# Kernel tuning notes

Hardware: AMD Instinct MI355X
Metric: run time of the kernel (lower is better)

Reference implementation:

```python
import jax, jax.numpy as jnp
import numpy as np

B, T, C = 2, 2048, 2048
HK, HV, DK, DV, KW = 16, 32, 128, 128, 4
KEY_DIM = HK * DK          # 2048
VAL_DIM = HV * DV          # 4096
QKV_DIM = 2 * KEY_DIM + VAL_DIM  # 8192
REPEAT = HV // HK
EPS = 1e-6


def setup_inputs() -> dict:
    key = jax.random.key(0)
    ks = jax.random.split(key, 12)
    s = 0.02
    return {
        "x": jax.random.normal(ks[0], (B, T, C), jnp.float32),
        "positions": jnp.arange(B * T, dtype=jnp.int64).reshape(B, T) % T,
        "W_qkv": jax.random.normal(ks[1], (QKV_DIM, C), jnp.float32) * s,
        "W_z": jax.random.normal(ks[2], (VAL_DIM, C), jnp.float32) * s,
        "W_b": jax.random.normal(ks[3], (HV, C), jnp.float32) * s,
        "W_a": jax.random.normal(ks[4], (HV, C), jnp.float32) * s,
        "conv_w": jax.random.normal(ks[5], (QKV_DIM, 1, KW), jnp.float32) * 0.3,
        "dt_bias": jnp.ones((HV,), jnp.float32),
        "A_log": jnp.log(jax.random.uniform(ks[6], (HV,), jnp.float32, 0.01, 16.0)),
        "norm_w": jnp.ones((DV,), jnp.float32),
        "W_out": jax.random.normal(ks[7], (C, VAL_DIM), jnp.float32) * s,
    }


def _forward(x, W_qkv, W_z, W_b, W_a, conv_w, dt_bias, A_log, norm_w, W_out):
    qkv = x @ W_qkv.T                                # [B,T,QKV_DIM]
    z = (x @ W_z.T).reshape(B, T, HV, DV)
    b = x @ W_b.T                                    # [B,T,HV]
    a = x @ W_a.T                                    # [B,T,HV]

    # depthwise causal conv1d (left pad KW-1), then SiLU
    qkv_c = jnp.transpose(qkv, (0, 2, 1))            # [B,QKV_DIM,T]
    qkv_c = jax.lax.conv_general_dilated(
        qkv_c, conv_w, window_strides=(1,), padding=[(KW - 1, 0)],
        dimension_numbers=("NCH", "OIH", "NCH"), feature_group_count=QKV_DIM)
    qkv = jax.nn.silu(jnp.transpose(qkv_c, (0, 2, 1)))

    q, k, v = jnp.split(qkv, [KEY_DIM, 2 * KEY_DIM], axis=-1)
    q = q.reshape(B, T, HK, DK)
    k = k.reshape(B, T, HK, DK)
    v = v.reshape(B, T, HV, DV)
    q = q / jnp.maximum(jnp.linalg.norm(q, axis=-1, keepdims=True), 1e-12)
    k = k / jnp.maximum(jnp.linalg.norm(k, axis=-1, keepdims=True), 1e-12)
    if REPEAT > 1:
        q = jnp.repeat(q, REPEAT, axis=2)            # [B,T,HV,DK]
        k = jnp.repeat(k, REPEAT, axis=2)

    beta = jax.nn.sigmoid(b)                         # [B,T,HV]
    g = -jnp.exp(A_log) * jax.nn.softplus(a + dt_bias)  # [B,T,HV]

    # gated delta-rule recurrence over time (lax.scan, time-major)
    def step(state, inp):
        g_t, beta_t, k_t, v_t, q_t = inp             # [B,HV], [B,HV], [B,HV,DK], [B,HV,DV], [B,HV,DK]
        state = jnp.exp(g_t)[..., None, None] * state \
            + beta_t[..., None, None] * (k_t[..., :, None] * v_t[..., None, :])
        out_t = jnp.einsum("bhk,bhkv->bhv", q_t, state)
        return state, out_t

    tm = lambda u: jnp.moveaxis(u, 1, 0)
    state0 = jnp.zeros((B, HV, DK, DV), x.dtype)
    _, out = jax.lax.scan(step, state0, (tm(g), tm(beta), tm(k), tm(v), tm(q)))
    out = jnp.moveaxis(out, 0, 1)                    # [B,T,HV,DV]

    # gated RMSNorm per head: RMSNorm(out) * silu(z)
    o = out.astype(jnp.float32)
    o = o * jax.lax.rsqrt(jnp.mean(o * o, axis=-1, keepdims=True) + EPS)
    o = (norm_w * o) * jax.nn.silu(z.astype(jnp.float32))
    o = o.astype(x.dtype).reshape(B, T, VAL_DIM)
    return o @ W_out.T                               # [B,T,C]


def reference(x, positions, W_qkv, W_z, W_b, W_a, conv_w, dt_bias, A_log, norm_w, W_out):
    del positions  # unused by the module's math
    return _forward(x, W_qkv, W_z, W_b, W_a, conv_w, dt_bias, A_log, norm_w, W_out)
```

## Files before the change

kernel.cpp:

```cpp
#include <hip/hip_runtime.h>

typedef unsigned short u16;
typedef unsigned int u32;
typedef __attribute__((ext_vector_type(8))) short short8;
typedef __attribute__((ext_vector_type(8))) _Float16 half8;
typedef __attribute__((ext_vector_type(4))) float f32x4;

#define NB 2
#define NT 2048
#define NC 2048
#define NHV 32
#define VALD 4096
#define NBT 4096
#define CL 64
#define NCH (NT / CL)

#define GL16(gp, lp) __builtin_amdgcn_global_load_lds( \
    (const __attribute__((address_space(1))) unsigned int*)(gp), \
    (__attribute__((address_space(3))) unsigned int*)(lp), 16, 0, 0)

static __device__ __forceinline__ float bf2f(u16 u) {
  union { u32 u; float f; } x; x.u = ((u32)u) << 16; return x.f;
}
static __device__ __forceinline__ u16 f2bf(float f) {
  union { float f; u32 u; } x; x.f = f;
  u32 r = x.u + 0x7fffu + ((x.u >> 16) & 1u);
  return (u16)(r >> 16);
}
static __device__ __forceinline__ u16 f2h(float f) {
  union { _Float16 h; u16 u; } c; c.h = (_Float16)f; return c.u;
}
static __device__ __forceinline__ float h2f(u16 u) {
  union { u16 u; _Float16 h; } c; c.u = u; return (float)c.h;
}
static __device__ __forceinline__ float sigm(float x) { return 1.0f / (1.0f + __expf(-x)); }
static __device__ __forceinline__ int ldsoff(int row, int c8) {
  return row * 48 + ((c8 ^ ((row >> 2) & 3)) << 3);
}

__global__ void k_sentinel(float* out) { out[0] = 1.0e6f; }

__global__ __launch_bounds__(256) void k_cvtx(const float* __restrict__ in, u16* __restrict__ hi,
                                              u16* __restrict__ lo, u16* __restrict__ h16, int n4) {
  int i = blockIdx.x * 256 + threadIdx.x;
  if (i >= n4) return;
  float4 v = ((const float4*)in)[i];
  ushort4 h, l, p;
  h.x = f2bf(v.x); l.x = f2bf(v.x - bf2f(h.x)); p.x = f2h(v.x);
  h.y = f2bf(v.y); l.y = f2bf(v.y - bf2f(h.y)); p.y = f2h(v.y);
  h.z = f2bf(v.z); l.z = f2bf(v.z - bf2f(h.z)); p.z = f2h(v.z);
  h.w = f2bf(v.w); l.w = f2bf(v.w - bf2f(h.w)); p.w = f2h(v.w);
  ((ushort4*)hi)[i] = h;
  ((ushort4*)lo)[i] = l;
  ((ushort4*)h16)[i] = p;
}

__global__ __launch_bounds__(256) void k_cvt16(const float* __restrict__ in, u16* __restrict__ out, int n4) {
  int i = blockIdx.x * 256 + threadIdx.x;
  if (i >= n4) return;
  float4 v = ((const float4*)in)[i];
  ushort4 o;
  o.x = f2h(v.x); o.y = f2h(v.y); o.z = f2h(v.z); o.w = f2h(v.w);
  ((ushort4*)out)[i] = o;
}

__global__ __launch_bounds__(256) void k_wba(const float* __restrict__ Wb, const float* __restrict__ Wa,
                                             u16* __restrict__ hi, u16* __restrict__ lo) {
  int i = blockIdx.x * 256 + threadIdx.x;
  int r = i >> 11, c = i & 2047;
  float v = 0.f;
  if (r < 32) v = Wb[r * 2048 + c];
  else if (r < 64) v = Wa[(r - 32) * 2048 + c];
  u16 h = f2bf(v);
  hi[i] = h;
  lo[i] = f2bf(v - bf2f(h));
}

__global__ __launch_bounds__(256) void k_gemm_bf3(const u16* __restrict__ Ahg, const u16* __restrict__ Alg,
                                                  const u16* __restrict__ Bhg, const u16* __restrict__ Blg,
                                                  float* __restrict__ C0, int M, int N, int K) {
  __shared__ __align__(16) u16 As_h[128 * 48];
  __shared__ __align__(16) u16 As_l[128 * 48];
  __shared__ __align__(16) u16 Bs_h[128 * 48];
  __shared__ __align__(16) u16 Bs_l[128 * 48];
  const int tid = threadIdx.x;
  const int lane = tid & 63, wave = tid >> 6;
  const int wr = wave >> 1, wc = wave & 1;
  const int l15 = lane & 15, l16 = lane >> 4;
  const int row0 = blockIdx.y * 128, col0 = blockIdx.x * 128;
  const int sr = tid >> 1, sk = (tid & 1) * 16;
  const int c0 = sk >> 3;
  const int w0 = ldsoff(sr, c0), w1 = ldsoff(sr, c0 + 1);
  f32x4 acc[4][4] = {};
  for (int k0 = 0; k0 < K; k0 += 32) {
    const size_t aoff = (size_t)(row0 + sr) * K + k0 + sk;
    const size_t boff = (size_t)(col0 + sr) * K + k0 + sk;
    *(short8*)&As_h[w0] = *(const short8*)&Ahg[aoff];
    *(short8*)&As_h[w1] = *(const short8*)&Ahg[aoff + 8];
    *(short8*)&As_l[w0] = *(const short8*)&Alg[aoff];
    *(short8*)&As_l[w1] = *(const short8*)&Alg[aoff + 8];
    *(short8*)&Bs_h[w0] = *(const short8*)&Bhg[boff];
    *(short8*)&Bs_h[w1] = *(const short8*)&Bhg[boff + 8];
    *(short8*)&Bs_l[w0] = *(const short8*)&Blg[boff];
    *(short8*)&Bs_l[w1] = *(const short8*)&Blg[boff + 8];
    __syncthreads();
    short8 ah[4], al[4], bh[4], bl[4];
#pragma unroll
    for (int mi = 0; mi < 4; ++mi) {
      int off = ldsoff(wr * 64 + mi * 16 + l15, l16);
      ah[mi] = *(short8*)&As_h[off];
      al[mi] = *(short8*)&As_l[off];
    }
#pragma unroll
    for (int ni = 0; ni < 4; ++ni) {
      int off = ldsoff(wc * 64 + ni * 16 + l15, l16);
      bh[ni] = *(short8*)&Bs_h[off];
      bl[ni] = *(short8*)&Bs_l[off];
    }
#pragma unroll
    for (int mi = 0; mi < 4; ++mi)
#pragma unroll
      for (int ni = 0; ni < 4; ++ni) {
        acc[mi][ni] = __builtin_amdgcn_mfma_f32_16x16x32_bf16(ah[mi], bh[ni], acc[mi][ni], 0, 0, 0);
        acc[mi][ni] = __builtin_amdgcn_mfma_f32_16x16x32_bf16(al[mi], bh[ni], acc[mi][ni], 0, 0, 0);
        acc[mi][ni] = __builtin_amdgcn_mfma_f32_16x16x32_bf16(ah[mi], bl[ni], acc[mi][ni], 0, 0, 0);
      }
    __syncthreads();
  }
#pragma unroll
  for (int mi = 0; mi < 4; ++mi)
#pragma unroll
    for (int ni = 0; ni < 4; ++ni) {
      int rr = row0 + wr * 64 + mi * 16 + l16 * 4;
      int cc = col0 + wc * 64 + ni * 16 + l15;
#pragma unroll
      for (int i = 0; i < 4; ++i)
        C0[(size_t)(rr + i) * N + cc] = acc[mi][ni][i];
    }
}

template <int MODE>
__global__ __launch_bounds__(256) void k_gemm16(const u16* __restrict__ Ag, const u16* __restrict__ Bg,
                                                void* __restrict__ C0, int M, int N, int K,
                                                const u16* __restrict__ e0, const float* __restrict__ e1,
                                                const float* __restrict__ e2) {
  __shared__ __align__(16) u16 As[2 * 128 * 64];
  __shared__ __align__(16) u16 Bs[2 * 128 * 64];
  const int tid = threadIdx.x;
  const int lane = tid & 63, wave = tid >> 6;
  const int wr = wave >> 1, wc = wave & 1;
  const int l15 = lane & 15, l16 = lane >> 4;
  const int row0 = blockIdx.y * 128, col0 = blockIdx.x * 128;
  u32 gA[4], gB[4], lofs[4];
#pragma unroll
  for (int i = 0; i < 4; ++i) {
    int o = wave * 2048 + i * 512 + lane * 8;
    int row = o >> 6;
    int cg = ((lane & 7) ^ (row & 7)) * 8;
    gA[i] = (u32)(row0 + row) * (u32)K + cg;
    gB[i] = (u32)(col0 + row) * (u32)K + cg;
    lofs[i] = (u32)(wave * 2048 + i * 512);
  }
  f32x4 acc[4][4] = {};
  const int NTILE = K >> 6;
#pragma unroll
  for (int i = 0; i < 4; ++i) {
    GL16(Ag + gA[i], &As[lofs[i]]);
    GL16(Bg + gB[i], &Bs[lofs[i]]);
  }
  for (int t = 0; t < NTILE; ++t) {
    const u32 cb = (u32)(t & 1) * 8192;
    __syncthreads();
    if (t + 1 < NTILE) {
      const u32 nb = cb ^ 8192;
      const int kn = (t + 1) << 6;
#pragma unroll
      for (int i = 0; i < 4; ++i) {
        GL16(Ag + gA[i] + kn, &As[nb + lofs[i]]);
        GL16(Bg + gB[i] + kn, &Bs[nb + lofs[i]]);
      }
    }
#pragma unroll
    for (int kk = 0; kk < 2; ++kk) {
      half8 a[4], b[4];
#pragma unroll
      for (int mi = 0; mi < 4; ++mi) {
        int row = wr * 64 + mi * 16 + l15;
        a[mi] = *(half8*)&As[cb + row * 64 + (((kk * 4 + l16) ^ (l15 & 7)) << 3)];
      }
#pragma unroll
      for (int ni = 0; ni < 4; ++ni) {
        int row = wc * 64 + ni * 16 + l15;
        b[ni] = *(half8*)&Bs[cb + row * 64 + (((kk * 4 + l16) ^ (l15 & 7)) << 3)];
      }
#pragma unroll
      for (int mi = 0; mi < 4; ++mi)
#pragma unroll
        for (int ni = 0; ni < 4; ++ni)
          acc[mi][ni] = __builtin_amdgcn_mfma_f32_16x16x32_f16(a[mi], b[ni], acc[mi][ni], 0, 0, 0);
    }
  }
#pragma unroll
  for (int mi = 0; mi < 4; ++mi) {
#pragma unroll
    for (int ni = 0; ni < 4; ++ni) {
      int rr = row0 + wr * 64 + mi * 16 + l16 * 4;
      int cc = col0 + wc * 64 + ni * 16 + l15;
#pragma unroll
      for (int i = 0; i < 4; ++i) {
        float v = acc[mi][ni][i];
        size_t idx = (size_t)(rr + i) * N + cc;
        if constexpr (MODE == 0) {
          ((float*)C0)[idx] = v;
        } else if constexpr (MODE == 1) {
          ((u16*)C0)[idx] = f2h(v);
        } else {
          float zs = v * sigm(v);
          float o = h2f(e0[idx]) * e1[(size_t)(rr + i) * 32 + (cc >> 7)] * e2[cc & 127] * zs;
          ((u16*)C0)[idx] = f2h(o);
        }
      }
    }
  }
}

__global__ __launch_bounds__(256) void k_bg(const float* __restrict__ ba, const float* __restrict__ dt_bias,
                                            const float* __restrict__ A_log, float* __restrict__ beta_t,
                                            float* __restrict__ g_t) {
  int i = blockIdx.x * 256 + threadIdx.x;
  int bt = i >> 5, h = i & 31;
  float bv = ba[(size_t)bt * 128 + h];
  float av = ba[(size_t)bt * 128 + 32 + h];
  beta_t[h * 4096 + bt] = sigm(bv);
  float xx = av + dt_bias[h];
  float sp = (xx > 20.f) ? xx : log1pf(__expf(xx));
  g_t[h * 4096 + bt] = -__expf(A_log[h]) * sp;
}

__global__ __launch_bounds__(256) void k_convqk(const u16* __restrict__ qkraw, const float* __restrict__ cw,
                                                u16* __restrict__ qkn) {
  __shared__ float sval[4096];
  __shared__ float snrm[32];
  const int tid = threadIdx.x;
  const int bt = blockIdx.x;
  const int b = bt >> 11, t = bt & 2047;
  for (int i = 0; i < 16; ++i) {
    int c = i * 256 + tid;
    float acc = 0.f;
#pragma unroll
    for (int j = 0; j < 4; ++j) {
      int ts = t - 3 + j;
      if (ts >= 0) acc += cw[c * 4 + j] * h2f(qkraw[(size_t)(b * 2048 + ts) * 4096 + c]);
    }
    sval[c] = acc * sigm(acc);
  }
  __syncthreads();
  {
    int gidx = tid >> 3, s = tid & 7;
    float ss = 0.f;
#pragma unroll
    for (int i2 = 0; i2 < 16; ++i2) { float v = sval[gidx * 128 + s * 16 + i2]; ss += v * v; }
    ss += __shfl_xor(ss, 1); ss += __shfl_xor(ss, 2); ss += __shfl_xor(ss, 4);
    if (s == 0) snrm[gidx] = 1.0f / fmaxf(sqrtf(ss), 1e-12f);
  }
  __syncthreads();
  for (int i = 0; i < 16; ++i) {
    int c = i * 256 + tid;
    qkn[(size_t)bt * 4096 + c] = f2h(sval[c] * snrm[c >> 7]);
  }
}

__global__ __launch_bounds__(512, 4) void k_scanc(const u16* __restrict__ qk16, const u16* __restrict__ v16,
                                                  const float* __restrict__ cw,
                                                  const float* __restrict__ beta_t, const float* __restrict__ g_t,
                                                  u16* __restrict__ outr) {
  __shared__ __align__(16) u16 Qs[64][136], Ks[64][136];
  __shared__ __align__(16) u16 Vs[32][72];
  __shared__ __align__(16) u16 SIs[64][72];
  __shared__ __align__(16) u16 SH[2][32][132];
  __shared__ u16 rv16[67][36];
  __shared__ float garr[64], barr[64], warr[64], earr[64];
  __shared__ float sdt;

  const int tid = threadIdx.x;
  const int lane = tid & 63, wv = tid >> 6;
  const int l15 = lane & 15, l16 = lane >> 4;
  const int dq = blockIdx.x & 3, h = (blockIdx.x >> 2) & 31, b = blockIdx.x >> 7;
  const int bT = b * 2048;
  const int hk = h >> 1;
  const int dvl = tid & 31;
  const int vch = h * 128 + dq * 32;
  const float4 cwv = *(const float4*)&cw[(4096 + vch + dvl) * 4];
  const int mblk = wv & 3, nh = wv >> 2;
  const int m0 = mblk * 16;
  const int sr = tid >> 3, d0 = (tid & 7) * 16;
  const int r0v = tid >> 5;

  for (int i = tid; i < 2 * 32 * 132; i += 512) ((u16*)SH)[i] = 0;
  f32x4 st[2] = {};

  short8 pq[2], pk[2];
  u16 pv[5];
  auto LOADQK = [&](int t0) {
    const size_t base = (size_t)(bT + t0 + sr) * 4096 + hk * 128 + d0;
    pq[0] = *(const short8*)&qk16[base];        pq[1] = *(const short8*)&qk16[base + 8];
    pk[0] = *(const short8*)&qk16[base + 2048]; pk[1] = *(const short8*)&qk16[base + 2056];
  };
  auto LOADV = [&](int t0) {
#pragma unroll
    for (int i = 0; i < 5; ++i) {
      int r = r0v + i * 16;
      int tr = t0 - 3 + r;
      pv[i] = (r < 67 && tr >= 0) ? v16[(size_t)(bT + tr) * 4096 + vch + dvl] : (u16)0;
    }
  };

  LOADQK(0);
  LOADV(0);

  for (int ch = 0; ch < NCH; ++ch) {
    const int t0 = ch * CL;
    const int p = ch & 1;
    *(short8*)&Qs[sr][d0] = pq[0]; *(short8*)&Qs[sr][d0 + 8] = pq[1];
    *(short8*)&Ks[sr][d0] = pk[0]; *(short8*)&Ks[sr][d0 + 8] = pk[1];
#pragma unroll
    for (int i = 0; i < 5; ++i) {
      int r = r0v + i * 16;
      if (r < 67) rv16[r][dvl] = pv[i];
    }
    if (wv == 0) {
      float gv = g_t[h * 4096 + bT + t0 + lane];
      float bv = beta_t[h * 4096 + bT + t0 + lane];
      float cum = gv;
#pragma unroll
      for (int off = 1; off < 64; off <<= 1) {
        float o = __shfl_up(cum, off);
        if (lane >= off) cum += o;
      }
      float tot = __shfl(cum, 63);
      garr[lane] = cum;
      earr[lane] = __expf(cum);
      warr[lane] = __expf(tot - cum) * bv;
      barr[lane] = bv;
      if (lane == 0) sdt = __expf(tot);
    }
    __syncthreads();
    if (ch + 1 < NCH) {
      LOADQK(t0 + CL);
      LOADV(t0 + CL);
    }
    {
      int tl = tid >> 5;
#pragma unroll
      for (int rr = 0; rr < 4; ++rr) {
        int t = rr * 16 + tl;
        float a = cwv.x * h2f(rv16[t][dvl]) + cwv.y * h2f(rv16[t + 1][dvl]) +
                  cwv.z * h2f(rv16[t + 2][dvl]) + cwv.w * h2f(rv16[t + 3][dvl]);
        a = a * sigm(a);
        Vs[dvl][t] = f2h(a);
      }
    }
    half8 a[4];
#pragma unroll
    for (int kk = 0; kk < 4; ++kk) a[kk] = *(half8*)&Qs[m0 + l15][l16 * 8 + kk * 32];
#pragma unroll
    for (int j = 0; j < 2; ++j) {
      int n = nh * 2 + j;
      f32x4 a4 = {};
#pragma unroll
      for (int kk = 0; kk < 4; ++kk) {
        half8 b8 = *(half8*)&Ks[n * 16 + l15][l16 * 8 + kk * 32];
        a4 = __builtin_amdgcn_mfma_f32_16x16x32_f16(a[kk], b8, a4, 0, 0, 0);
      }
      int col = n * 16 + l15;
      float gc = garr[col], bc = barr[col];
#pragma unroll
      for (int i = 0; i < 4; ++i) {
        int row = m0 + l16 * 4 + i;
        float cval = (col <= row) ? __expf(garr[row] - gc) * bc * a4[i] : 0.f;
        SIs[row][col] = f2h(cval);
      }
    }
    __syncthreads();
    f32x4 ao = {};
#pragma unroll
    for (int kk = 0; kk < 4; ++kk) {
      half8 s8 = *(half8*)&SH[p][nh * 16 + l15][l16 * 8 + kk * 32];
      ao = __builtin_amdgcn_mfma_f32_16x16x32_f16(a[kk], s8, ao, 0, 0, 0);
    }
#pragma unroll
    for (int i = 0; i < 4; ++i) ao[i] *= earr[m0 + l16 * 4 + i];
#pragma unroll
    for (int kk = 0; kk < 2; ++kk) {
      half8 asi = *(half8*)&SIs[m0 + l15][l16 * 8 + kk * 32];
      half8 bv8 = *(half8*)&Vs[nh * 16 + l15][l16 * 8 + kk * 32];
      ao = __builtin_amdgcn_mfma_f32_16x16x32_f16(asi, bv8, ao, 0, 0, 0);
    }
#pragma unroll
    for (int i = 0; i < 4; ++i)
      outr[(size_t)(bT + t0 + m0 + l16 * 4 + i) * 4096 + vch + nh * 16 + l15] = f2h(ao[i]);
#pragma unroll
    for (int m = 0; m < 2; ++m)
#pragma unroll
      for (int i = 0; i < 4; ++i) st[m][i] *= sdt;
#pragma unroll
    for (int kk = 0; kk < 2; ++kk) {
      half8 bw;
      {
        int dk = wv * 16 + l15;
#pragma unroll
        for (int e = 0; e < 8; ++e) {
          int s = l16 * 8 + e + kk * 32;
          bw[e] = (_Float16)(h2f(Ks[s][dk]) * warr[s]);
        }
      }
#pragma unroll
      for (int m = 0; m < 2; ++m) {
        half8 av = *(half8*)&Vs[m * 16 + l15][l16 * 8 + kk * 32];
        st[m] = __builtin_amdgcn_mfma_f32_16x16x32_f16(av, bw, st[m], 0, 0, 0);
      }
    }
#pragma unroll
    for (int m = 0; m < 2; ++m)
#pragma unroll
      for (int i = 0; i < 4; ++i)
        SH[p ^ 1][m * 16 + l16 * 4 + i][wv * 16 + l15] = f2h(st[m][i]);
    __syncthreads();
  }
}

__global__ __launch_bounds__(256) void k_rms(const u16* __restrict__ outr, float* __restrict__ rms) {
  int pair = blockIdx.x * 4 + (threadIdx.x >> 6);
  int lane = threadIdx.x & 63;
  u32 pv = *(const u32*)&outr[(size_t)pair * 128 + lane * 2];
  float v0 = h2f((u16)pv), v1 = h2f((u16)(pv >> 16));
  float ss = v0 * v0 + v1 * v1;
#pragma unroll
  for (int m = 1; m < 64; m <<= 1) ss += __shfl_xor(ss, m);
  if (lane == 0) rms[pair] = rsqrtf(ss * (1.0f / 128.0f) + 1e-6f);
}

extern "C" void kernel_launch(void* const* d_in, const int* in_sizes, int n_in,
                              void* d_out, int out_size, void* d_ws, size_t ws_size,
                              hipStream_t stream) {
  const float* x = (const float*)d_in[0];
  const float* W_qkv = (const float*)d_in[2];
  const float* W_z = (const float*)d_in[3];
  const float* W_b = (const float*)d_in[4];
  const float* W_a = (const float*)d_in[5];
  const float* conv_w = (const float*)d_in[6];
  const float* dt_bias = (const float*)d_in[7];
  const float* A_log = (const float*)d_in[8];
  const float* norm_w = (const float*)d_in[9];
  const float* W_out = (const float*)d_in[10];
  float* out = (float*)d_out;

  const size_t MB = 1ull << 20;
  const size_t need = 192 * MB + 3 * (size_t)NBT * 32 * 4;
  if (ws_size < need) {
    k_sentinel<<<1, 1, 0, stream>>>(out);
    return;
  }
  char* ws = (char*)d_ws;
  u16* xh = (u16*)ws;
  u16* xl = (u16*)(ws + 16 * MB);
  u16* xh16 = (u16*)(ws + 32 * MB);
  u16* wz16 = (u16*)(ws + 48 * MB);
  u16* qkB16 = (u16*)(ws + 64 * MB);
  u16* wout16 = (u16*)(ws + 64 * MB);
  u16* qkA16 = (u16*)(ws + 96 * MB);
  u16* om16 = (u16*)(ws + 96 * MB);
  u16* wsh16 = (u16*)(ws + 128 * MB);
  u16* outr16 = (u16*)(ws + 128 * MB);
  u16* v16 = (u16*)(ws + 160 * MB);
  u16* wbah = (u16*)(ws + 160 * MB);
  u16* wbal = (u16*)(ws + 160 * MB + 512 * 1024);
  float* babuf = (float*)(ws + 161 * MB);
  float* beta_t = (float*)(ws + 192 * MB);
  float* g_t = beta_t + (size_t)NBT * 32;
  float* rmsb = g_t + (size_t)NBT * 32;

  const int N4X = NBT * NC / 4;
  k_cvtx<<<N4X / 256, 256, 0, stream>>>(x, xh, xl, xh16, N4X);
  k_cvt16<<<2 * N4X / 256, 256, 0, stream>>>(W_qkv, wsh16, 2 * N4X);
  k_cvt16<<<N4X / 256, 256, 0, stream>>>(W_z, wz16, N4X);
  k_wba<<<128 * NC / 256, 256, 0, stream>>>(W_b, W_a, wbah, wbal);
  k_gemm_bf3<<<dim3(1, NBT / 128), 256, 0, stream>>>(xh, xl, wbah, wbal, babuf, NBT, 128, NC);
  k_bg<<<NBT * 32 / 256, 256, 0, stream>>>(babuf, dt_bias, A_log, beta_t, g_t);

  k_gemm16<1><<<dim3(4096 / 128, NBT / 128), 256, 0, stream>>>(xh16, wsh16, qkA16, NBT, 4096, NC,
                                                               nullptr, nullptr, nullptr);
  k_convqk<<<NBT, 256, 0, stream>>>(qkA16, conv_w, qkB16);

  k_gemm16<1><<<dim3(4096 / 128, NBT / 128), 256, 0, stream>>>(xh16, wsh16 + (size_t)4096 * NC, v16,
                                                               NBT, 4096, NC, nullptr, nullptr, nullptr);

  k_scanc<<<256, 512, 0, stream>>>(qkB16, v16, conv_w, beta_t, g_t, outr16);
  k_rms<<<NBT * NHV / 4, 256, 0, stream>>>(outr16, rmsb);

  k_gemm16<2><<<dim3(VALD / 128, NBT / 128), 256, 0, stream>>>(xh16, wz16, om16, NBT, VALD, NC,
                                                               outr16, rmsb, norm_w);

  k_cvt16<<<N4X / 256, 256, 0, stream>>>(W_out, wout16, N4X);
  k_gemm16<0><<<dim3(NC / 128, NBT / 128), 256, 0, stream>>>(om16, wout16, out, NBT, NC, VALD,
                                                             nullptr, nullptr, nullptr);
}
```

Measured before the change: 657.6 us.

## Swizzle GEMM block order across XCDs and prefetch scan gate cumsum

The GEMM launches become a 1D grid whose block index is remapped so consecutive tiles land on the same XCD (blockIdx mod 8), with the intent of improving L2 reuse of A/B tiles. Separately, the chunked scan kernel double-buffers its gate/beta cumsum arrays: the g/beta loads for the next chunk are issued early and the wave-0 cumsum runs at the end of the current chunk instead of at the start. This removes the serial cumsum from the critical path before the first barrier. The swizzle assumes the grid size is a multiple of 8, and the cumsum change adds a little shared memory and some registers.

Result: faster. 644.2 us (-2.0%).

```diff
diff --git a/kernel.cpp b/kernel.cpp
--- a/kernel.cpp
+++ b/kernel.cpp
@@ -150,7 +150,10 @@
   const int lane = tid & 63, wave = tid >> 6;
   const int wr = wave >> 1, wc = wave & 1;
   const int l15 = lane & 15, l16 = lane >> 4;
-  const int row0 = blockIdx.y * 128, col0 = blockIdx.x * 128;
+  const int qx = gridDim.x >> 3;
+  const int swz = ((int)blockIdx.x & 7) * qx + ((int)blockIdx.x >> 3);
+  const int nbx = N >> 7;
+  const int row0 = (swz / nbx) * 128, col0 = (swz % nbx) * 128;
   u32 gA[4], gB[4], lofs[4];
 #pragma unroll
   for (int i = 0; i < 4; ++i) {
@@ -279,8 +282,8 @@
   __shared__ __align__(16) u16 SIs[64][72];
   __shared__ __align__(16) u16 SH[2][32][132];
   __shared__ u16 rv16[67][36];
-  __shared__ float garr[64], barr[64], warr[64], earr[64];
-  __shared__ float sdt;
+  __shared__ float garr[2][64], barr[2][64], warr[2][64], earr[2][64];
+  __shared__ float sdt[2];
 
   const int tid = threadIdx.x;
   const int lane = tid & 63, wv = tid >> 6;
@@ -301,6 +304,7 @@
 
   short8 pq[2], pk[2];
   u16 pv[5];
+  float pgv, pbv;
   auto LOADQK = [&](int t0) {
     const size_t base = (size_t)(bT + t0 + sr) * 4096 + hk * 128 + d0;
     pq[0] = *(const short8*)&qk16[base];        pq[1] = *(const short8*)&qk16[base + 8];
@@ -314,9 +318,28 @@
       pv[i] = (r < 67 && tr >= 0) ? v16[(size_t)(bT + tr) * 4096 + vch + dvl] : (u16)0;
     }
   };
+  auto CUMSUM = [&](float gv, float bv, int buf) {
+    float cum = gv;
+#pragma unroll
+    for (int off = 1; off < 64; off <<= 1) {
+      float o = __shfl_up(cum, off);
+      if (lane >= off) cum += o;
+    }
+    float tot = __shfl(cum, 63);
+    garr[buf][lane] = cum;
+    earr[buf][lane] = __expf(cum);
+    warr[buf][lane] = __expf(tot - cum) * bv;
+    barr[buf][lane] = bv;
+    if (lane == 0) sdt[buf] = __expf(tot);
+  };
 
   LOADQK(0);
   LOADV(0);
+  if (wv == 0) {
+    float gv = g_t[h * 4096 + bT + lane];
+    float bv = beta_t[h * 4096 + bT + lane];
+    CUMSUM(gv, bv, 0);
+  }
 
   for (int ch = 0; ch < NCH; ++ch) {
     const int t0 = ch * CL;
@@ -328,26 +351,14 @@
       int r = r0v + i * 16;
       if (r < 67) rv16[r][dvl] = pv[i];
     }
-    if (wv == 0) {
-      float gv = g_t[h * 4096 + bT + t0 + lane];
-      float bv = beta_t[h * 4096 + bT + t0 + lane];
-      float cum = gv;
-#pragma unroll
-      for (int off = 1; off < 64; off <<= 1) {
-        float o = __shfl_up(cum, off);
-        if (lane >= off) cum += o;
-      }
-      float tot = __shfl(cum, 63);
-      garr[lane] = cum;
-      earr[lane] = __expf(cum);
-      warr[lane] = __expf(tot - cum) * bv;
-      barr[lane] = bv;
-      if (lane == 0) sdt = __expf(tot);
-    }
     __syncthreads();
     if (ch + 1 < NCH) {
       LOADQK(t0 + CL);
       LOADV(t0 + CL);
+      if (wv == 0) {
+        pgv = g_t[h * 4096 + bT + t0 + CL + lane];
+        pbv = beta_t[h * 4096 + bT + t0 + CL + lane];
+      }
     }
     {
       int tl = tid >> 5;
@@ -373,11 +384,11 @@
         a4 = __builtin_amdgcn_mfma_f32_16x16x32_f16(a[kk], b8, a4, 0, 0, 0);
       }
       int col = n * 16 + l15;
-      float gc = garr[col], bc = barr[col];
+      float gc = garr[p][col], bc = barr[p][col];
 #pragma unroll
       for (int i = 0; i < 4; ++i) {
         int row = m0 + l16 * 4 + i;
-        float cval = (col <= row) ? __expf(garr[row] - gc) * bc * a4[i] : 0.f;
+        float cval = (col <= row) ? __expf(garr[p][row] - gc) * bc * a4[i] : 0.f;
         SIs[row][col] = f2h(cval);
       }
     }
@@ -389,7 +400,7 @@
       ao = __builtin_amdgcn_mfma_f32_16x16x32_f16(a[kk], s8, ao, 0, 0, 0);
     }
 #pragma unroll
-    for (int i = 0; i < 4; ++i) ao[i] *= earr[m0 + l16 * 4 + i];
+    for (int i = 0; i < 4; ++i) ao[i] *= earr[p][m0 + l16 * 4 + i];
 #pragma unroll
     for (int kk = 0; kk < 2; ++kk) {
       half8 asi = *(half8*)&SIs[m0 + l15][l16 * 8 + kk * 32];
@@ -399,10 +410,11 @@
 #pragma unroll
     for (int i = 0; i < 4; ++i)
       outr[(size_t)(bT + t0 + m0 + l16 * 4 + i) * 4096 + vch + nh * 16 + l15] = f2h(ao[i]);
+    const float sd = sdt[p];
 #pragma unroll
     for (int m = 0; m < 2; ++m)
 #pragma unroll
-      for (int i = 0; i < 4; ++i) st[m][i] *= sdt;
+      for (int i = 0; i < 4; ++i) st[m][i] *= sd;
 #pragma unroll
     for (int kk = 0; kk < 2; ++kk) {
       half8 bw;
@@ -411,7 +423,7 @@
 #pragma unroll
         for (int e = 0; e < 8; ++e) {
           int s = l16 * 8 + e + kk * 32;
-          bw[e] = (_Float16)(h2f(Ks[s][dk]) * warr[s]);
+          bw[e] = (_Float16)(h2f(Ks[s][dk]) * warr[p][s]);
         }
       }
 #pragma unroll
@@ -425,6 +437,7 @@
 #pragma unroll
       for (int i = 0; i < 4; ++i)
         SH[p ^ 1][m * 16 + l16 * 4 + i][wv * 16 + l15] = f2h(st[m][i]);
+    if (wv == 0 && ch + 1 < NCH) CUMSUM(pgv, pbv, p ^ 1);
     __syncthreads();
   }
 }
@@ -488,20 +501,20 @@
   k_gemm_bf3<<<dim3(1, NBT / 128), 256, 0, stream>>>(xh, xl, wbah, wbal, babuf, NBT, 128, NC);
   k_bg<<<NBT * 32 / 256, 256, 0, stream>>>(babuf, dt_bias, A_log, beta_t, g_t);
 
-  k_gemm16<1><<<dim3(4096 / 128, NBT / 128), 256, 0, stream>>>(xh16, wsh16, qkA16, NBT, 4096, NC,
-                                                               nullptr, nullptr, nullptr);
+  k_gemm16<1><<<(NBT / 128) * (4096 / 128), 256, 0, stream>>>(xh16, wsh16, qkA16, NBT, 4096, NC,
+                                                              nullptr, nullptr, nullptr);
   k_convqk<<<NBT, 256, 0, stream>>>(qkA16, conv_w, qkB16);
 
-  k_gemm16<1><<<dim3(4096 / 128, NBT / 128), 256, 0, stream>>>(xh16, wsh16 + (size_t)4096 * NC, v16,
-                                                               NBT, 4096, NC, nullptr, nullptr, nullptr);
+  k_gemm16<1><<<(NBT / 128) * (4096 / 128), 256, 0, stream>>>(xh16, wsh16 + (size_t)4096 * NC, v16,
+                                                              NBT, 4096, NC, nullptr, nullptr, nullptr);
 
   k_scanc<<<256, 512, 0, stream>>>(qkB16, v16, conv_w, beta_t, g_t, outr16);
   k_rms<<<NBT * NHV / 4, 256, 0, stream>>>(outr16, rmsb);
 
-  k_gemm16<2><<<dim3(VALD / 128, NBT / 128), 256, 0, stream>>>(xh16, wz16, om16, NBT, VALD, NC,
-                                                               outr16, rmsb, norm_w);
+  k_gemm16<2><<<(NBT / 128) * (VALD / 128), 256, 0, stream>>>(xh16, wz16, om16, NBT, VALD, NC,
+                                                              outr16, rmsb, norm_w);
 
   k_cvt16<<<N4X / 256, 256, 0, stream>>>(W_out, wout16, N4X);
-  k_gemm16<0><<<dim3(NC / 128, NBT / 128), 256, 0, stream>>>(om16, wout16, out, NBT, NC, VALD,
-                                                             nullptr, nullptr, nullptr);
-}
+  k_gemm16<0><<<(NBT / 128) * (NC / 128), 256, 0, stream>>>(om16, wout16, out, NBT, NC, VALD,
+                                                            nullptr, nullptr, nullptr);
+}
```
